# Kernel tuning notes

Hardware: AMD Instinct MI355X
Metric: run time of the kernel (lower is better)

Reference implementation:

```python
import jax, jax.numpy as jnp
import numpy as np

HEADS = 12
EPS_RMS = 1e-6
EPS_LN = 1e-5


def _rms_inorm(x, w):
    # torch.std over spatial dims (unbiased, ddof=1); no mean subtraction
    std = jnp.std(x, axis=(2, 3), keepdims=True, ddof=1)
    return x / (std + EPS_RMS) * w[None, :, None, None]


def _layernorm(x, w, b):
    m = jnp.mean(x, axis=-1, keepdims=True)
    v = jnp.var(x, axis=-1, keepdims=True)
    return (x - m) / jnp.sqrt(v + EPS_LN) * w + b


def setup_inputs() -> dict:
    key = jax.random.key(0)
    ks = jax.random.split(key, 16)
    B, C, H, W = 8, 768, 64, 64
    hd = C // HEADS
    s = 0.02
    return {
        "x": jax.random.normal(ks[0], (B, C, H, W), jnp.float32),
        "bcs": jnp.zeros((1, 2), jnp.int32),
        "norm1_w": jnp.ones((C,), jnp.float32),
        "norm2_w": jnp.ones((C,), jnp.float32),
        "mlpn_w": jnp.ones((C,), jnp.float32),
        "Win": jax.random.normal(ks[1], (3 * C, C), jnp.float32) * s,
        "bin_": jnp.zeros((3 * C,), jnp.float32),
        "Wout": jax.random.normal(ks[2], (C, C), jnp.float32) * s,
        "bout": jnp.zeros((C,), jnp.float32),
        "qn_w": jnp.ones((hd,), jnp.float32),
        "qn_b": jnp.zeros((hd,), jnp.float32),
        "kn_w": jnp.ones((hd,), jnp.float32),
        "kn_b": jnp.zeros((hd,), jnp.float32),
        "gamma_att": jnp.full((C,), 1e-6, jnp.float32),
        "gamma_mlp": jnp.full((C,), 1e-6, jnp.float32),
        "W1": jax.random.normal(ks[3], (C, 4 * C), jnp.float32) * s,
        "b1": jnp.zeros((4 * C,), jnp.float32),
        "W2": jax.random.normal(ks[4], (4 * C, C), jnp.float32) * s,
        "b2": jnp.zeros((C,), jnp.float32),
    }


def reference(x, bcs, norm1_w, norm2_w, mlpn_w, Win, bin_, Wout, bout,
              qn_w, qn_b, kn_w, kn_b, gamma_att, gamma_mlp, W1, b1, W2, b2):
    B, C, H, W = x.shape
    hd = C // HEADS
    scale = 1.0 / jnp.sqrt(jnp.asarray(hd, x.dtype))

    h = _rms_inorm(x, norm1_w)
    # 1x1 conv QKV: [B, 3C, H, W]
    qkv = jnp.einsum('bchw,oc->bohw', h, Win) + bin_[None, :, None, None]
    # b (he c3) h w -> b he h w c3, then split into q,k,v of head_dim each
    qkv = qkv.reshape(B, HEADS, 3 * hd, H, W).transpose(0, 1, 3, 4, 2)
    q, k, v = jnp.split(qkv, 3, axis=-1)  # each [B, he, H, W, hd]
    q = _layernorm(q, qn_w, qn_b)
    k = _layernorm(k, kn_w, kn_b)

    # row attention: attend along W for each row h
    sx = jnp.einsum('bnhqc,bnhkc->bnhqk', q, k) * scale
    xx = jnp.einsum('bnhqk,bnhkc->bnhqc', jax.nn.softmax(sx, axis=-1), v)
    # column attention: attend along H for each column w
    sy = jnp.einsum('bnqwc,bnkwc->bnwqk', q, k) * scale
    xy = jnp.einsum('bnwqk,bnkwc->bnqwc', jax.nn.softmax(sy, axis=-1), v)

    a = (xx + xy) * 0.5  # [B, he, H, W, hd]
    a = a.transpose(0, 1, 4, 2, 3).reshape(B, C, H, W)
    a = _rms_inorm(a, norm2_w)
    a = jnp.einsum('bchw,oc->bohw', a, Wout) + bout[None, :, None, None]
    x1 = a * gamma_att[None, :, None, None] + x

    t = x1.transpose(0, 2, 3, 1)  # [B, H, W, C]
    m = jax.nn.gelu(t @ W1 + b1, approximate=False) @ W2 + b2
    m = m.transpose(0, 3, 1, 2)
    m = _rms_inorm(m, mlpn_w)
    return x1 + gamma_mlp[None, :, None, None] * m
```

## Files before the change

kernel.cpp:

```cpp
#include <hip/hip_runtime.h>

typedef __attribute__((ext_vector_type(8))) short short8;
typedef __attribute__((ext_vector_type(4))) float f32x4;
typedef __attribute__((ext_vector_type(4))) unsigned short u16x4;
typedef __attribute__((ext_vector_type(8))) unsigned short u16x8;

#define BDIM 8
#define CDIM 768
#define C3 2304
#define C4 3072
#define HEADS 12
#define HD 64
#define HWD 4096
#define TOKS 32768

__device__ __forceinline__ float bf2f(unsigned short u) {
    union { unsigned int i; float f; } x; x.i = ((unsigned int)u) << 16; return x.f;
}
__device__ __forceinline__ unsigned short f2bf(float f) {
    union { float f; unsigned int i; } x; x.f = f;
    unsigned int r = x.i + 0x7FFFu + ((x.i >> 16) & 1u);
    return (unsigned short)(r >> 16);
}

__device__ __forceinline__ void gload_lds16(const unsigned short* g, unsigned short* l) {
    __builtin_amdgcn_global_load_lds(
        (const __attribute__((address_space(1))) void*)g,
        (__attribute__((address_space(3))) void*)l, 16, 0, 0);
}

__global__ __launch_bounds__(256) void convert_f32_bf16(
    const float* __restrict__ src, unsigned short* __restrict__ dst, int n)
{
    int i = (blockIdx.x * 256 + threadIdx.x) * 4;
    if (i + 3 >= n + 4) return;
    if (i + 3 < n) {
        float4 v = *(const float4*)&src[i];
        dst[i + 0] = f2bf(v.x); dst[i + 1] = f2bf(v.y);
        dst[i + 2] = f2bf(v.z); dst[i + 3] = f2bf(v.w);
    }
}

__global__ __launch_bounds__(256) void transpose_w(
    const float* __restrict__ src, unsigned short* __restrict__ dst, int R, int Cc)
{
    const int n0 = blockIdx.x * 64, k0 = blockIdx.y * 64;
    __shared__ float t[64][65];
    #pragma unroll
    for (int s = 0; s < 16; ++s) {
        int flat = threadIdx.x + 256 * s;
        int i = flat >> 6, j = flat & 63;
        t[i][j] = src[(long)(k0 + i) * Cc + n0 + j];
    }
    __syncthreads();
    #pragma unroll
    for (int s = 0; s < 16; ++s) {
        int flat = threadIdx.x + 256 * s;
        int jn = flat >> 6, ik = flat & 63;
        dst[(long)(n0 + jn) * R + k0 + ik] = f2bf(t[ik][jn]);
    }
}

__global__ __launch_bounds__(256) void stats_spatial_f32(
    const float* __restrict__ x, const float* __restrict__ wgt,
    float* __restrict__ sout, float eps)
{
    const int bc = blockIdx.x;
    const int c = bc % CDIM;
    const float4* p4 = (const float4*)(x + (long)bc * HWD);
    float s = 0.f, ss = 0.f;
    #pragma unroll
    for (int k = 0; k < 4; ++k) {
        float4 v = p4[threadIdx.x + 256 * k];
        s  += v.x + v.y + v.z + v.w;
        ss += v.x * v.x + v.y * v.y + v.z * v.z + v.w * v.w;
    }
    #pragma unroll
    for (int m = 1; m < 64; m <<= 1) { s += __shfl_xor(s, m); ss += __shfl_xor(ss, m); }
    __shared__ float rs[4], rss[4];
    int w = threadIdx.x >> 6, lane = threadIdx.x & 63;
    if (lane == 0) { rs[w] = s; rss[w] = ss; }
    __syncthreads();
    if (threadIdx.x == 0) {
        float S = rs[0] + rs[1] + rs[2] + rs[3];
        float Q = rss[0] + rss[1] + rss[2] + rss[3];
        float var = (Q - S * S * (1.f / 4096.f)) * (1.f / 4095.f);
        sout[bc] = wgt[c] / (sqrtf(var) + eps);
    }
}

__global__ __launch_bounds__(256) void stats_spatial_bf16(
    const unsigned short* __restrict__ t, const float* __restrict__ wgt,
    float* __restrict__ sout, float eps)
{
    const int b = blockIdx.x / 12, cg = blockIdx.x % 12;
    const int sub = threadIdx.x & 15, tr = threadIdx.x >> 4;
    const unsigned short* base = t + (long)b * HWD * CDIM + cg * 64 + sub * 4;
    float s[4] = {0.f, 0.f, 0.f, 0.f}, q[4] = {0.f, 0.f, 0.f, 0.f};
    for (int i = 0; i < 256; ++i) {
        const int token = tr + 16 * i;
        u16x4 v = *(const u16x4*)(base + (long)token * CDIM);
        #pragma unroll
        for (int j = 0; j < 4; ++j) { float f = bf2f(v[j]); s[j] += f; q[j] += f * f; }
    }
    __shared__ float ssum[16][64], ssq[16][64];
    #pragma unroll
    for (int j = 0; j < 4; ++j) { ssum[tr][sub * 4 + j] = s[j]; ssq[tr][sub * 4 + j] = q[j]; }
    __syncthreads();
    if (threadIdx.x < 64) {
        const int c = threadIdx.x;
        float S = 0.f, Q = 0.f;
        #pragma unroll
        for (int r = 0; r < 16; ++r) { S += ssum[r][c]; Q += ssq[r][c]; }
        const float var = (Q - S * S * (1.f / 4096.f)) * (1.f / 4095.f);
        const int cglob = cg * 64 + c;
        sout[b * CDIM + cglob] = wgt[cglob] / (sqrtf(var) + eps);
    }
}

__global__ __launch_bounds__(256) void make_h(
    const float* __restrict__ x, const float* __restrict__ s1,
    unsigned short* __restrict__ h)
{
    const int hw0 = blockIdx.x * 64, c0 = blockIdx.y * 64, b = blockIdx.z;
    __shared__ float t[64][65];
    #pragma unroll
    for (int s = 0; s < 16; ++s) {
        int flat = threadIdx.x + 256 * s;
        int ci = flat >> 6, hj = flat & 63;
        t[ci][hj] = x[(long)(b * CDIM + c0 + ci) * HWD + hw0 + hj];
    }
    __syncthreads();
    #pragma unroll
    for (int s = 0; s < 16; ++s) {
        int flat = threadIdx.x + 256 * s;
        int hi = flat >> 6, cj = flat & 63;
        float v = t[cj][hi] * s1[b * CDIM + c0 + cj];
        h[(long)(b * HWD + hw0 + hi) * CDIM + c0 + cj] = f2bf(v);
    }
}

template<int GELU>
__global__ __launch_bounds__(256) void gemm_bt(
    const unsigned short* __restrict__ A, const unsigned short* __restrict__ BT,
    const float* __restrict__ bias, unsigned short* __restrict__ out,
    int M, int N, int K)
{
    __shared__ unsigned short sA[128 * 32];
    __shared__ unsigned short sB[128 * 32];
    const int tid = threadIdx.x;
    const int lane = tid & 63, w = tid >> 6;
    const int wm = w >> 1, wn = w & 1;
    const int m0 = blockIdx.x * 128, n0 = blockIdx.y * 128;
    const int lr = lane & 15, lk = (lane >> 4) << 3;

    const int r0 = tid >> 2, kk0 = (tid & 3) << 3;
    const int r1 = (tid + 256) >> 2, kk1 = (tid & 3) << 3;
    const int ldsOff0 = (w << 6) * 8;
    const int ldsOff1 = ((w << 6) + 256) * 8;

    f32x4 acc[4][4] = {};

    for (int kb = 0; kb < K; kb += 32) {
        gload_lds16(&A[(long)(m0 + r0) * K + kb + kk0], &sA[ldsOff0]);
        gload_lds16(&A[(long)(m0 + r1) * K + kb + kk1], &sA[ldsOff1]);
        gload_lds16(&BT[(long)(n0 + r0) * K + kb + kk0], &sB[ldsOff0]);
        gload_lds16(&BT[(long)(n0 + r1) * K + kb + kk1], &sB[ldsOff1]);
        __syncthreads();
        short8 af[4], bf8[4];
        #pragma unroll
        for (int mi = 0; mi < 4; ++mi) af[mi] = *(const short8*)&sA[((wm * 64 + mi * 16 + lr) << 5) + lk];
        #pragma unroll
        for (int ni = 0; ni < 4; ++ni) bf8[ni] = *(const short8*)&sB[((wn * 64 + ni * 16 + lr) << 5) + lk];
        #pragma unroll
        for (int mi = 0; mi < 4; ++mi)
            #pragma unroll
            for (int ni = 0; ni < 4; ++ni)
                acc[mi][ni] = __builtin_amdgcn_mfma_f32_16x16x32_bf16(af[mi], bf8[ni], acc[mi][ni], 0, 0, 0);
        __syncthreads();
    }

    const int er = (lane >> 4) << 2;
    #pragma unroll
    for (int mi = 0; mi < 4; ++mi) {
        #pragma unroll
        for (int ni = 0; ni < 4; ++ni) {
            const int gcol = n0 + wn * 64 + ni * 16 + lr;
            const float bv = bias[gcol];
            #pragma unroll
            for (int r = 0; r < 4; ++r) {
                const int grow = m0 + wm * 64 + mi * 16 + er + r;
                float v = acc[mi][ni][r] + bv;
                if (GELU) v = 0.5f * v * (1.f + erff(v * 0.70710678118f));
                out[(long)grow * N + gcol] = f2bf(v);
            }
        }
    }
}

__global__ __launch_bounds__(256) void qk_layernorm(
    unsigned short* __restrict__ qkv,
    const float* __restrict__ qw, const float* __restrict__ qb,
    const float* __restrict__ kw, const float* __restrict__ kb)
{
    const int pairIdx = blockIdx.x * 16 + (threadIdx.x >> 4);
    const int token = pairIdx / HEADS, he = pairIdx % HEADS;
    const int c4 = (threadIdx.x & 15) * 4;
    const long base = (long)token * C3 + he * 192;
    #pragma unroll
    for (int which = 0; which < 2; ++which) {
        const long off = base + which * 64 + c4;
        u16x4 v = *(u16x4*)&qkv[off];
        float f[4];
        #pragma unroll
        for (int j = 0; j < 4; ++j) f[j] = bf2f(v[j]);
        float s = f[0] + f[1] + f[2] + f[3];
        float q = f[0] * f[0] + f[1] * f[1] + f[2] * f[2] + f[3] * f[3];
        #pragma unroll
        for (int m = 1; m < 16; m <<= 1) { s += __shfl_xor(s, m); q += __shfl_xor(q, m); }
        const float mean = s * (1.f / 64.f);
        const float var = q * (1.f / 64.f) - mean * mean;
        const float rstd = rsqrtf(var + 1e-5f);
        const float* W = which ? kw : qw;
        const float* Bv = which ? kb : qb;
        u16x4 o;
        #pragma unroll
        for (int j = 0; j < 4; ++j)
            o[j] = f2bf((f[j] - mean) * rstd * W[c4 + j] + Bv[c4 + j]);
        *(u16x4*)&qkv[off] = o;
    }
}

template<int AXIS>
__global__ __launch_bounds__(128) void attn_axial(
    const unsigned short* __restrict__ qkv, unsigned short* __restrict__ a)
{
    __shared__ unsigned short lds[2][2][64 * 72];
    const int tid = threadIdx.x;
    const int lane = tid & 63, w = tid >> 6;
    const int lineG = blockIdx.x * 2 + w;
    const int b = lineG / 768;
    const int rem = lineG - b * 768;
    const int he = rem >> 6, line = rem & 63;
    const int ts = (AXIS == 0) ? 1 : 64;
    const long token0 = (long)b * HWD + (AXIS == 0 ? line * 64 : line);
    const long qbase = token0 * C3 + he * 192;
    unsigned short* VT = &lds[w][0][0];
    unsigned short* P  = &lds[w][1][0];
    const int lr = lane & 15, g = lane >> 4;

    {
        const int keyr = lane >> 3, d8 = (lane & 7) << 3;
        #pragma unroll
        for (int it = 0; it < 8; ++it) {
            const int key = it * 8 + keyr;
            u16x8 v = *(const u16x8*)&qkv[qbase + (long)key * ts * C3 + 128 + d8];
            #pragma unroll
            for (int j = 0; j < 8; ++j) VT[(d8 + j) * 72 + key] = v[j];
        }
    }

    short8 qf[4][2], kf[4][2];
    #pragma unroll
    for (int i = 0; i < 4; ++i)
        #pragma unroll
        for (int kk = 0; kk < 2; ++kk) {
            const long rb = qbase + (long)(i * 16 + lr) * ts * C3 + kk * 32 + g * 8;
            qf[i][kk] = *(const short8*)&qkv[rb];
            kf[i][kk] = *(const short8*)&qkv[rb + 64];
        }

    f32x4 acc[4][4] = {};
    #pragma unroll
    for (int mi = 0; mi < 4; ++mi)
        #pragma unroll
        for (int ni = 0; ni < 4; ++ni) {
            acc[mi][ni] = __builtin_amdgcn_mfma_f32_16x16x32_bf16(qf[mi][0], kf[ni][0], acc[mi][ni], 0, 0, 0);
            acc[mi][ni] = __builtin_amdgcn_mfma_f32_16x16x32_bf16(qf[mi][1], kf[ni][1], acc[mi][ni], 0, 0, 0);
        }

    #pragma unroll
    for (int mi = 0; mi < 4; ++mi)
        #pragma unroll
        for (int r = 0; r < 4; ++r) {
            float mx = -1e30f;
            #pragma unroll
            for (int ni = 0; ni < 4; ++ni) {
                float v = acc[mi][ni][r] * 0.125f; acc[mi][ni][r] = v; mx = fmaxf(mx, v);
            }
            #pragma unroll
            for (int m = 1; m < 16; m <<= 1) mx = fmaxf(mx, __shfl_xor(mx, m));
            float s = 0.f;
            #pragma unroll
            for (int ni = 0; ni < 4; ++ni) {
                float e = __expf(acc[mi][ni][r] - mx); acc[mi][ni][r] = e; s += e;
            }
            #pragma unroll
            for (int m = 1; m < 16; m <<= 1) s += __shfl_xor(s, m);
            const float inv = 1.f / s;
            const int row = mi * 16 + 4 * g + r;
            #pragma unroll
            for (int ni = 0; ni < 4; ++ni)
                P[row * 72 + ni * 16 + lr] = f2bf(acc[mi][ni][r] * inv);
        }
    __syncthreads();

    short8 pa[4][2], vb[4][2];
    #pragma unroll
    for (int i = 0; i < 4; ++i)
        #pragma unroll
        for (int kk = 0; kk < 2; ++kk) {
            pa[i][kk] = *(const short8*)&P[(i * 16 + lr) * 72 + kk * 32 + g * 8];
            vb[i][kk] = *(const short8*)&VT[(i * 16 + lr) * 72 + kk * 32 + g * 8];
        }
    f32x4 o2[4][4] = {};
    #pragma unroll
    for (int mi = 0; mi < 4; ++mi)
        #pragma unroll
        for (int ni = 0; ni < 4; ++ni) {
            o2[mi][ni] = __builtin_amdgcn_mfma_f32_16x16x32_bf16(pa[mi][0], vb[ni][0], o2[mi][ni], 0, 0, 0);
            o2[mi][ni] = __builtin_amdgcn_mfma_f32_16x16x32_bf16(pa[mi][1], vb[ni][1], o2[mi][ni], 0, 0, 0);
        }

    #pragma unroll
    for (int mi = 0; mi < 4; ++mi)
        #pragma unroll
        for (int r = 0; r < 4; ++r) {
            const int q = mi * 16 + 4 * g + r;
            const long tok = token0 + (long)q * ts;
            #pragma unroll
            for (int ni = 0; ni < 4; ++ni) {
                const int d = ni * 16 + lr;
                const long addr = tok * CDIM + he * 64 + d;
                const float v = o2[mi][ni][r] * 0.5f;
                if (AXIS == 0) a[addr] = f2bf(v);
                else           a[addr] = f2bf(bf2f(a[addr]) + v);
            }
        }
}

__global__ __launch_bounds__(256) void scale_inplace(
    unsigned short* __restrict__ a, const float* __restrict__ s2)
{
    const long i = ((long)blockIdx.x * 256 + threadIdx.x) * 4;
    const int c = (int)(i % CDIM);
    const int b = (int)(i / ((long)CDIM * HWD));
    u16x4 v = *(u16x4*)&a[i];
    u16x4 o;
    #pragma unroll
    for (int j = 0; j < 4; ++j) o[j] = f2bf(bf2f(v[j]) * s2[b * CDIM + c + j]);
    *(u16x4*)&a[i] = o;
}

__global__ __launch_bounds__(256) void x1_combine(
    const unsigned short* __restrict__ o, const float* __restrict__ x,
    const float* __restrict__ gamma, float* __restrict__ dout,
    unsigned short* __restrict__ x1b)
{
    const int hw0 = blockIdx.x * 64, c0 = blockIdx.y * 64, b = blockIdx.z;
    __shared__ float t[64][65];
    #pragma unroll
    for (int s = 0; s < 16; ++s) {
        int flat = threadIdx.x + 256 * s;
        int i = flat >> 6, j = flat & 63;
        t[i][j] = bf2f(o[(long)(b * HWD + hw0 + i) * CDIM + c0 + j]);
    }
    __syncthreads();
    #pragma unroll
    for (int s = 0; s < 16; ++s) {
        int flat = threadIdx.x + 256 * s;
        int j = flat >> 6, i = flat & 63;
        const long xi = (long)(b * CDIM + c0 + j) * HWD + hw0 + i;
        float v = x[xi] + gamma[c0 + j] * t[i][j];
        dout[xi] = v;
        t[i][j] = v;
    }
    __syncthreads();
    #pragma unroll
    for (int s = 0; s < 16; ++s) {
        int flat = threadIdx.x + 256 * s;
        int i = flat >> 6, j = flat & 63;
        x1b[(long)(b * HWD + hw0 + i) * CDIM + c0 + j] = f2bf(t[i][j]);
    }
}

__global__ __launch_bounds__(256) void final_combine(
    const unsigned short* __restrict__ m, const float* __restrict__ gm,
    const float* __restrict__ s3, float* __restrict__ dout)
{
    const int hw0 = blockIdx.x * 64, c0 = blockIdx.y * 64, b = blockIdx.z;
    __shared__ float t[64][65];
    #pragma unroll
    for (int s = 0; s < 16; ++s) {
        int flat = threadIdx.x + 256 * s;
        int i = flat >> 6, j = flat & 63;
        t[i][j] = bf2f(m[(long)(b * HWD + hw0 + i) * CDIM + c0 + j]);
    }
    __syncthreads();
    #pragma unroll
    for (int s = 0; s < 16; ++s) {
        int flat = threadIdx.x + 256 * s;
        int j = flat >> 6, i = flat & 63;
        const long xi = (long)(b * CDIM + c0 + j) * HWD + hw0 + i;
        dout[xi] = dout[xi] + gm[c0 + j] * s3[b * CDIM + c0 + j] * t[i][j];
    }
}

extern "C" void kernel_launch(void* const* d_in, const int* in_sizes, int n_in,
                              void* d_out, int out_size, void* d_ws, size_t ws_size,
                              hipStream_t stream) {
    const float* x      = (const float*)d_in[0];
    const float* n1w    = (const float*)d_in[2];
    const float* n2w    = (const float*)d_in[3];
    const float* mlw    = (const float*)d_in[4];
    const float* Win    = (const float*)d_in[5];
    const float* bin    = (const float*)d_in[6];
    const float* Wout   = (const float*)d_in[7];
    const float* bout   = (const float*)d_in[8];
    const float* qn_w   = (const float*)d_in[9];
    const float* qn_b   = (const float*)d_in[10];
    const float* kn_w   = (const float*)d_in[11];
    const float* kn_b   = (const float*)d_in[12];
    const float* gatt   = (const float*)d_in[13];
    const float* gmlp   = (const float*)d_in[14];
    const float* W1     = (const float*)d_in[15];
    const float* b1     = (const float*)d_in[16];
    const float* W2     = (const float*)d_in[17];
    const float* b2     = (const float*)d_in[18];
    float* dout = (float*)d_out;
    char* ws = (char*)d_ws;

    unsigned short* wQ  = (unsigned short*)(ws);
    unsigned short* wO  = (unsigned short*)(ws + (4L << 20));
    unsigned short* w1t = (unsigned short*)(ws + (6L << 20));
    unsigned short* w2t = (unsigned short*)(ws + (11L << 20));
    float* s1 = (float*)(ws + (16L << 20));
    float* s2 = s1 + 6144;
    float* s3 = s2 + 6144;
    unsigned short* bufH = (unsigned short*)(ws + (17L << 20));
    unsigned short* bufQ = (unsigned short*)(ws + (65L << 20));
    unsigned short* bufA = (unsigned short*)(ws + (209L << 20));

    convert_f32_bf16<<<1728, 256, 0, stream>>>(Win, wQ, C3 * CDIM);
    convert_f32_bf16<<<576, 256, 0, stream>>>(Wout, wO, CDIM * CDIM);
    transpose_w<<<dim3(C4 / 64, CDIM / 64), 256, 0, stream>>>(W1, w1t, CDIM, C4);
    transpose_w<<<dim3(CDIM / 64, C4 / 64), 256, 0, stream>>>(W2, w2t, C4, CDIM);

    stats_spatial_f32<<<BDIM * CDIM, 256, 0, stream>>>(x, n1w, s1, 1e-6f);
    make_h<<<dim3(64, 12, 8), 256, 0, stream>>>(x, s1, bufH);

    gemm_bt<0><<<dim3(TOKS / 128, C3 / 128), 256, 0, stream>>>(bufH, wQ, bin, bufQ, TOKS, C3, CDIM);
    qk_layernorm<<<TOKS * HEADS / 16, 256, 0, stream>>>(bufQ, qn_w, qn_b, kn_w, kn_b);

    attn_axial<0><<<BDIM * HEADS * 64 / 2, 128, 0, stream>>>(bufQ, bufA);
    attn_axial<1><<<BDIM * HEADS * 64 / 2, 128, 0, stream>>>(bufQ, bufA);

    stats_spatial_bf16<<<BDIM * 12, 256, 0, stream>>>(bufA, n2w, s2, 1e-6f);
    scale_inplace<<<TOKS * CDIM / 1024, 256, 0, stream>>>(bufA, s2);
    gemm_bt<0><<<dim3(TOKS / 128, CDIM / 128), 256, 0, stream>>>(bufA, wO, bout, bufH, TOKS, CDIM, CDIM);
    x1_combine<<<dim3(64, 12, 8), 256, 0, stream>>>(bufH, x, gatt, dout, bufA);

    for (int ch = 0; ch < 2; ++ch) {
        const unsigned short* x1c = bufA + (long)ch * 16384 * CDIM;
        unsigned short* mc = bufH + (long)ch * 16384 * CDIM;
        gemm_bt<1><<<dim3(16384 / 128, C4 / 128), 256, 0, stream>>>(x1c, w1t, b1, bufQ, 16384, C4, CDIM);
        gemm_bt<0><<<dim3(16384 / 128, CDIM / 128), 256, 0, stream>>>(bufQ, w2t, b2, mc, 16384, CDIM, C4);
    }

    stats_spatial_bf16<<<BDIM * 12, 256, 0, stream>>>(bufH, mlw, s3, 1e-6f);
    final_combine<<<dim3(64, 12, 8), 256, 0, stream>>>(bufH, gmlp, s3, dout);
}
```

Baseline: 1.089 ms.

## Replace bf16 GEMM with 256x256 tile, 4-stage LDS pipeline and swizzled layout

Replaces the 128x128 single-buffered GEMM with a 256x256-tile, 512-thread kernel that prefetches three K-slices ahead into a 4-slot LDS ring using explicit vmcnt waits. It adds an XOR swizzle on LDS rows to cut bank conflicts, raises MFMA priority with s_setprio, and remaps block IDs so neighbouring workgroups share A/B tiles in cache. The aim is to hide global-load latency and raise arithmetic intensity in all four projection GEMMs. The cost is 128 KB of dynamic LDS per block and more register pressure, which lowers occupancy.

```diff
diff --git a/kernel.cpp b/kernel.cpp
--- a/kernel.cpp
+++ b/kernel.cpp
@@ -141,55 +141,103 @@
 }
 
 template<int GELU>
-__global__ __launch_bounds__(256) void gemm_bt(
+__global__ __launch_bounds__(512, 2) void gemm256(
     const unsigned short* __restrict__ A, const unsigned short* __restrict__ BT,
     const float* __restrict__ bias, unsigned short* __restrict__ out,
     int M, int N, int K)
 {
-    __shared__ unsigned short sA[128 * 32];
-    __shared__ unsigned short sB[128 * 32];
+    extern __shared__ unsigned short smem[];
     const int tid = threadIdx.x;
     const int lane = tid & 63, w = tid >> 6;
-    const int wm = w >> 1, wn = w & 1;
-    const int m0 = blockIdx.x * 128, n0 = blockIdx.y * 128;
-    const int lr = lane & 15, lk = (lane >> 4) << 3;
-
-    const int r0 = tid >> 2, kk0 = (tid & 3) << 3;
-    const int r1 = (tid + 256) >> 2, kk1 = (tid & 3) << 3;
-    const int ldsOff0 = (w << 6) * 8;
-    const int ldsOff1 = ((w << 6) + 256) * 8;
-
-    f32x4 acc[4][4] = {};
-
-    for (int kb = 0; kb < K; kb += 32) {
-        gload_lds16(&A[(long)(m0 + r0) * K + kb + kk0], &sA[ldsOff0]);
-        gload_lds16(&A[(long)(m0 + r1) * K + kb + kk1], &sA[ldsOff1]);
-        gload_lds16(&BT[(long)(n0 + r0) * K + kb + kk0], &sB[ldsOff0]);
-        gload_lds16(&BT[(long)(n0 + r1) * K + kb + kk1], &sB[ldsOff1]);
-        __syncthreads();
-        short8 af[4], bf8[4];
-        #pragma unroll
-        for (int mi = 0; mi < 4; ++mi) af[mi] = *(const short8*)&sA[((wm * 64 + mi * 16 + lr) << 5) + lk];
-        #pragma unroll
-        for (int ni = 0; ni < 4; ++ni) bf8[ni] = *(const short8*)&sB[((wn * 64 + ni * 16 + lr) << 5) + lk];
+    const int wm = w >> 2, wn = w & 3;
+    const int lr = lane & 15, g = lane >> 4;
+
+    const int nwg = gridDim.x;
+    const int logical = (blockIdx.x & 7) * (nwg >> 3) + (blockIdx.x >> 3);
+    const int gmx = M >> 8;
+    const int m0 = (logical % gmx) << 8;
+    const int n0 = (logical / gmx) << 8;
+
+    const int ka = (((tid & 3) ^ ((tid >> 3) & 3)) << 3);
+    const int rA0 = tid >> 2, rA1 = (512 + tid) >> 2;
+    const unsigned short* aS0 = A + (long)(m0 + rA0) * K + ka;
+    const unsigned short* aS1 = A + (long)(m0 + rA1) * K + ka;
+    const unsigned short* bS0 = BT + (long)(n0 + rA0) * K + ka;
+    const unsigned short* bS1 = BT + (long)(n0 + rA1) * K + ka;
+    unsigned short* dA0 = smem + ((tid & ~63) + 0) * 8;
+    unsigned short* dA1 = smem + ((tid & ~63) + 512) * 8;
+    unsigned short* dB0 = dA0 + 32768;
+    unsigned short* dB1 = dA1 + 32768;
+
+#define STAGE(slot) do { \
+        gload_lds16(aS0, dA0 + (slot) * 8192); \
+        gload_lds16(aS1, dA1 + (slot) * 8192); \
+        gload_lds16(bS0, dB0 + (slot) * 8192); \
+        gload_lds16(bS1, dB1 + (slot) * 8192); \
+        aS0 += 32; aS1 += 32; bS0 += 32; bS1 += 32; } while (0)
+
+    const int nsub = K >> 5;
+    const int koff = ((g ^ ((lr >> 1) & 3)) << 3);
+    const int arow = wm * 128 + lr;
+    const int brow = wn * 64 + lr;
+
+    f32x4 acc[8][4] = {};
+
+    STAGE(0); STAGE(1); STAGE(2);
+    asm volatile("s_waitcnt vmcnt(8)" ::: "memory");
+    __builtin_amdgcn_s_barrier();
+
+    for (int j = 0; j < nsub; ++j) {
+        const int slot = j & 3;
+        const unsigned short* aT = smem + slot * 8192;
+        const unsigned short* bT = smem + 32768 + slot * 8192;
+
+        short8 af[4], bf[4];
+        #pragma unroll
+        for (int mi = 0; mi < 4; ++mi) af[mi] = *(const short8*)&aT[(arow + mi * 16) * 32 + koff];
+        #pragma unroll
+        for (int ni = 0; ni < 4; ++ni) bf[ni] = *(const short8*)&bT[(brow + ni * 16) * 32 + koff];
+        if (j + 3 < nsub) STAGE((j + 3) & 3);
+        __builtin_amdgcn_s_barrier();
+        asm volatile("s_waitcnt lgkmcnt(0)" ::: "memory");
+        __builtin_amdgcn_s_setprio(1);
         #pragma unroll
         for (int mi = 0; mi < 4; ++mi)
             #pragma unroll
             for (int ni = 0; ni < 4; ++ni)
-                acc[mi][ni] = __builtin_amdgcn_mfma_f32_16x16x32_bf16(af[mi], bf8[ni], acc[mi][ni], 0, 0, 0);
-        __syncthreads();
-    }
-
-    const int er = (lane >> 4) << 2;
-    #pragma unroll
-    for (int mi = 0; mi < 4; ++mi) {
+                acc[mi][ni] = __builtin_amdgcn_mfma_f32_16x16x32_bf16(af[mi], bf[ni], acc[mi][ni], 0, 0, 0);
+        __builtin_amdgcn_s_setprio(0);
+        __builtin_amdgcn_s_barrier();
+
+        short8 ag[4];
+        #pragma unroll
+        for (int mi = 0; mi < 4; ++mi) ag[mi] = *(const short8*)&aT[(arow + (mi + 4) * 16) * 32 + koff];
+        __builtin_amdgcn_s_barrier();
+        asm volatile("s_waitcnt lgkmcnt(0)" ::: "memory");
+        __builtin_amdgcn_s_setprio(1);
+        #pragma unroll
+        for (int mi = 0; mi < 4; ++mi)
+            #pragma unroll
+            for (int ni = 0; ni < 4; ++ni)
+                acc[mi + 4][ni] = __builtin_amdgcn_mfma_f32_16x16x32_bf16(ag[mi], bf[ni], acc[mi + 4][ni], 0, 0, 0);
+        __builtin_amdgcn_s_setprio(0);
+        const int rem = nsub - 2 - j;
+        if (rem >= 2)      { asm volatile("s_waitcnt vmcnt(8)" ::: "memory"); }
+        else if (rem == 1) { asm volatile("s_waitcnt vmcnt(4)" ::: "memory"); }
+        else if (rem == 0) { asm volatile("s_waitcnt vmcnt(0)" ::: "memory"); }
+        __builtin_amdgcn_s_barrier();
+    }
+#undef STAGE
+
+    #pragma unroll
+    for (int mi = 0; mi < 8; ++mi) {
         #pragma unroll
         for (int ni = 0; ni < 4; ++ni) {
             const int gcol = n0 + wn * 64 + ni * 16 + lr;
             const float bv = bias[gcol];
             #pragma unroll
             for (int r = 0; r < 4; ++r) {
-                const int grow = m0 + wm * 64 + mi * 16 + er + r;
+                const int grow = m0 + wm * 128 + mi * 16 + g * 4 + r;
                 float v = acc[mi][ni][r] + bv;
                 if (GELU) v = 0.5f * v * (1.f + erff(v * 0.70710678118f));
                 out[(long)grow * N + gcol] = f2bf(v);
@@ -441,6 +489,9 @@
     unsigned short* bufQ = (unsigned short*)(ws + (65L << 20));
     unsigned short* bufA = (unsigned short*)(ws + (209L << 20));
 
+    hipFuncSetAttribute((const void*)&gemm256<0>, hipFuncAttributeMaxDynamicSharedMemorySize, 131072);
+    hipFuncSetAttribute((const void*)&gemm256<1>, hipFuncAttributeMaxDynamicSharedMemorySize, 131072);
+
     convert_f32_bf16<<<1728, 256, 0, stream>>>(Win, wQ, C3 * CDIM);
     convert_f32_bf16<<<576, 256, 0, stream>>>(Wout, wO, CDIM * CDIM);
     transpose_w<<<dim3(C4 / 64, CDIM / 64), 256, 0, stream>>>(W1, w1t, CDIM, C4);
@@ -449,7 +500,7 @@
     stats_spatial_f32<<<BDIM * CDIM, 256, 0, stream>>>(x, n1w, s1, 1e-6f);
     make_h<<<dim3(64, 12, 8), 256, 0, stream>>>(x, s1, bufH);
 
-    gemm_bt<0><<<dim3(TOKS / 128, C3 / 128), 256, 0, stream>>>(bufH, wQ, bin, bufQ, TOKS, C3, CDIM);
+    gemm256<0><<<(TOKS / 256) * (C3 / 256), 512, 131072, stream>>>(bufH, wQ, bin, bufQ, TOKS, C3, CDIM);
     qk_layernorm<<<TOKS * HEADS / 16, 256, 0, stream>>>(bufQ, qn_w, qn_b, kn_w, kn_b);
 
     attn_axial<0><<<BDIM * HEADS * 64 / 2, 128, 0, stream>>>(bufQ, bufA);
@@ -457,14 +508,14 @@
 
     stats_spatial_bf16<<<BDIM * 12, 256, 0, stream>>>(bufA, n2w, s2, 1e-6f);
     scale_inplace<<<TOKS * CDIM / 1024, 256, 0, stream>>>(bufA, s2);
-    gemm_bt<0><<<dim3(TOKS / 128, CDIM / 128), 256, 0, stream>>>(bufA, wO, bout, bufH, TOKS, CDIM, CDIM);
+    gemm256<0><<<(TOKS / 256) * (CDIM / 256), 512, 131072, stream>>>(bufA, wO, bout, bufH, TOKS, CDIM, CDIM);
     x1_combine<<<dim3(64, 12, 8), 256, 0, stream>>>(bufH, x, gatt, dout, bufA);
 
     for (int ch = 0; ch < 2; ++ch) {
         const unsigned short* x1c = bufA + (long)ch * 16384 * CDIM;
         unsigned short* mc = bufH + (long)ch * 16384 * CDIM;
-        gemm_bt<1><<<dim3(16384 / 128, C4 / 128), 256, 0, stream>>>(x1c, w1t, b1, bufQ, 16384, C4, CDIM);
-        gemm_bt<0><<<dim3(16384 / 128, CDIM / 128), 256, 0, stream>>>(bufQ, w2t, b2, mc, 16384, CDIM, C4);
+        gemm256<1><<<(16384 / 256) * (C4 / 256), 512, 131072, stream>>>(x1c, w1t, b1, bufQ, 16384, C4, CDIM);
+        gemm256<0><<<(16384 / 256) * (CDIM / 256), 512, 131072, stream>>>(bufQ, w2t, b2, mc, 16384, CDIM, C4);
     }
 
     stats_spatial_bf16<<<BDIM * 12, 256, 0, stream>>>(bufH, mlw, s3, 1e-6f);
```

New measurement: 1.031 ms. 5.3% less time.

## Replace GEMM with 256x128 tile, double-buffered LDS pipeline and XCD-aware block remap

Applied to the files above, without the earlier changes.

Replaces the 128x128 single-buffered GEMM with a 512-thread kernel computing a 256x128 tile. It uses two LDS stages so the next k-slice is fetched while MFMAs run on the current one, XOR-swizzles the LDS layout to avoid bank conflicts, raises wave priority around the MFMA block, and remaps the 1D grid so neighbouring tiles share cache across XCDs. This is meant to hide global-load latency and improve operand reuse in all four GEMMs. In exchange it relies on hand-placed waitcnt and barriers and more LDS per block, which could lower occupancy or introduce ordering bugs.

```diff
diff --git a/kernel.cpp b/kernel.cpp
--- a/kernel.cpp
+++ b/kernel.cpp
@@ -141,46 +141,76 @@
 }
 
 template<int GELU>
-__global__ __launch_bounds__(256) void gemm_bt(
+__global__ __launch_bounds__(512, 4) void gemm256(
     const unsigned short* __restrict__ A, const unsigned short* __restrict__ BT,
     const float* __restrict__ bias, unsigned short* __restrict__ out,
     int M, int N, int K)
 {
-    __shared__ unsigned short sA[128 * 32];
-    __shared__ unsigned short sB[128 * 32];
+    extern __shared__ unsigned short smem[];
     const int tid = threadIdx.x;
     const int lane = tid & 63, w = tid >> 6;
     const int wm = w >> 1, wn = w & 1;
-    const int m0 = blockIdx.x * 128, n0 = blockIdx.y * 128;
-    const int lr = lane & 15, lk = (lane >> 4) << 3;
-
-    const int r0 = tid >> 2, kk0 = (tid & 3) << 3;
-    const int r1 = (tid + 256) >> 2, kk1 = (tid & 3) << 3;
-    const int ldsOff0 = (w << 6) * 8;
-    const int ldsOff1 = ((w << 6) + 256) * 8;
+    const int lr = lane & 15, g = lane >> 4;
+
+    const int nwg = gridDim.x;
+    const int logical = (blockIdx.x & 7) * (nwg >> 3) + (blockIdx.x >> 3);
+    const int gnx = N >> 7;
+    const int n0 = (logical % gnx) << 7;
+    const int m0 = (logical / gnx) << 8;
+
+    const int ka = (((tid & 3) ^ ((tid >> 3) & 3)) << 3);
+    const unsigned short* aS0 = A + (long)(m0 + (tid >> 2)) * K + ka;
+    const unsigned short* aS1 = A + (long)(m0 + 128 + (tid >> 2)) * K + ka;
+    const unsigned short* bS = BT + (long)(n0 + (tid >> 2)) * K + ka;
+    unsigned short* dA0 = smem + (tid & ~63) * 8;
+    unsigned short* dA1 = dA0 + 4096;
+    unsigned short* dB  = smem + 16384 + (tid & ~63) * 8;
+
+#define GSTAGE(S) do { \
+        gload_lds16(aS0, dA0 + (S) * 8192); \
+        gload_lds16(aS1, dA1 + (S) * 8192); \
+        gload_lds16(bS,  dB  + (S) * 4096); \
+        aS0 += 32; aS1 += 32; bS += 32; } while (0)
+
+    const int nsub = K >> 5;
+    const int koff = ((g ^ ((lr >> 1) & 3)) << 3);
+    const unsigned short* baseA = smem + (wm * 64 + lr) * 32 + koff;
+    const unsigned short* baseB = smem + 16384 + (wn * 64 + lr) * 32 + koff;
 
     f32x4 acc[4][4] = {};
 
-    for (int kb = 0; kb < K; kb += 32) {
-        gload_lds16(&A[(long)(m0 + r0) * K + kb + kk0], &sA[ldsOff0]);
-        gload_lds16(&A[(long)(m0 + r1) * K + kb + kk1], &sA[ldsOff1]);
-        gload_lds16(&BT[(long)(n0 + r0) * K + kb + kk0], &sB[ldsOff0]);
-        gload_lds16(&BT[(long)(n0 + r1) * K + kb + kk1], &sB[ldsOff1]);
-        __syncthreads();
-        short8 af[4], bf8[4];
-        #pragma unroll
-        for (int mi = 0; mi < 4; ++mi) af[mi] = *(const short8*)&sA[((wm * 64 + mi * 16 + lr) << 5) + lk];
-        #pragma unroll
-        for (int ni = 0; ni < 4; ++ni) bf8[ni] = *(const short8*)&sB[((wn * 64 + ni * 16 + lr) << 5) + lk];
-        #pragma unroll
-        for (int mi = 0; mi < 4; ++mi)
-            #pragma unroll
-            for (int ni = 0; ni < 4; ++ni)
-                acc[mi][ni] = __builtin_amdgcn_mfma_f32_16x16x32_bf16(af[mi], bf8[ni], acc[mi][ni], 0, 0, 0);
-        __syncthreads();
-    }
-
-    const int er = (lane >> 4) << 2;
+    GSTAGE(0); GSTAGE(1);
+
+#define SUBTILE(U, STG, WAITN) do { \
+        asm volatile("s_waitcnt vmcnt(" #WAITN ")" ::: "memory"); \
+        __builtin_amdgcn_s_barrier(); \
+        short8 bf[4], af[4]; \
+        _Pragma("unroll") \
+        for (int ni = 0; ni < 4; ++ni) bf[ni] = *(const short8*)(baseB + (U) * 4096 + ni * 512); \
+        _Pragma("unroll") \
+        for (int mi = 0; mi < 4; ++mi) af[mi] = *(const short8*)(baseA + (U) * 8192 + mi * 512); \
+        asm volatile("s_waitcnt lgkmcnt(0)" ::: "memory"); \
+        __builtin_amdgcn_s_barrier(); \
+        __builtin_amdgcn_sched_barrier(0); \
+        STG; \
+        __builtin_amdgcn_s_setprio(1); \
+        _Pragma("unroll") \
+        for (int mi = 0; mi < 4; ++mi) \
+            _Pragma("unroll") \
+            for (int ni = 0; ni < 4; ++ni) \
+                acc[mi][ni] = __builtin_amdgcn_mfma_f32_16x16x32_bf16(af[mi], bf[ni], acc[mi][ni], 0, 0, 0); \
+        __builtin_amdgcn_s_setprio(0); \
+        __builtin_amdgcn_sched_barrier(0); } while (0)
+
+    for (int j2 = 0; j2 + 2 < nsub; j2 += 2) {
+        SUBTILE(0, GSTAGE(0), 3);
+        SUBTILE(1, GSTAGE(1), 3);
+    }
+    SUBTILE(0, , 3);
+    SUBTILE(1, , 0);
+#undef SUBTILE
+#undef GSTAGE
+
     #pragma unroll
     for (int mi = 0; mi < 4; ++mi) {
         #pragma unroll
@@ -189,7 +219,7 @@
             const float bv = bias[gcol];
             #pragma unroll
             for (int r = 0; r < 4; ++r) {
-                const int grow = m0 + wm * 64 + mi * 16 + er + r;
+                const int grow = m0 + wm * 64 + mi * 16 + g * 4 + r;
                 float v = acc[mi][ni][r] + bv;
                 if (GELU) v = 0.5f * v * (1.f + erff(v * 0.70710678118f));
                 out[(long)grow * N + gcol] = f2bf(v);
@@ -449,7 +479,7 @@
     stats_spatial_f32<<<BDIM * CDIM, 256, 0, stream>>>(x, n1w, s1, 1e-6f);
     make_h<<<dim3(64, 12, 8), 256, 0, stream>>>(x, s1, bufH);
 
-    gemm_bt<0><<<dim3(TOKS / 128, C3 / 128), 256, 0, stream>>>(bufH, wQ, bin, bufQ, TOKS, C3, CDIM);
+    gemm256<0><<<(TOKS / 256) * (C3 / 128), 512, 49152, stream>>>(bufH, wQ, bin, bufQ, TOKS, C3, CDIM);
     qk_layernorm<<<TOKS * HEADS / 16, 256, 0, stream>>>(bufQ, qn_w, qn_b, kn_w, kn_b);
 
     attn_axial<0><<<BDIM * HEADS * 64 / 2, 128, 0, stream>>>(bufQ, bufA);
@@ -457,14 +487,14 @@
 
     stats_spatial_bf16<<<BDIM * 12, 256, 0, stream>>>(bufA, n2w, s2, 1e-6f);
     scale_inplace<<<TOKS * CDIM / 1024, 256, 0, stream>>>(bufA, s2);
-    gemm_bt<0><<<dim3(TOKS / 128, CDIM / 128), 256, 0, stream>>>(bufA, wO, bout, bufH, TOKS, CDIM, CDIM);
+    gemm256<0><<<(TOKS / 256) * (CDIM / 128), 512, 49152, stream>>>(bufA, wO, bout, bufH, TOKS, CDIM, CDIM);
     x1_combine<<<dim3(64, 12, 8), 256, 0, stream>>>(bufH, x, gatt, dout, bufA);
 
     for (int ch = 0; ch < 2; ++ch) {
         const unsigned short* x1c = bufA + (long)ch * 16384 * CDIM;
         unsigned short* mc = bufH + (long)ch * 16384 * CDIM;
-        gemm_bt<1><<<dim3(16384 / 128, C4 / 128), 256, 0, stream>>>(x1c, w1t, b1, bufQ, 16384, C4, CDIM);
-        gemm_bt<0><<<dim3(16384 / 128, CDIM / 128), 256, 0, stream>>>(bufQ, w2t, b2, mc, 16384, CDIM, C4);
+        gemm256<1><<<(16384 / 256) * (C4 / 128), 512, 49152, stream>>>(x1c, w1t, b1, bufQ, 16384, C4, CDIM);
+        gemm256<0><<<(16384 / 256) * (CDIM / 128), 512, 49152, stream>>>(bufQ, w2t, b2, mc, 16384, CDIM, C4);
     }
 
     stats_spatial_bf16<<<BDIM * 12, 256, 0, stream>>>(bufH, mlw, s3, 1e-6f);
```

After: 923.1 us, median of 2. 15.2% less time.
